# Optimization experiments

Hardware: AMD Instinct MI355X
Metric: run time of the kernel (lower is better)

## Reference

```python
import jax, jax.numpy as jnp
import numpy as np
from jax import lax

B, C, H, W = 8, 36, 256, 256
E, K, TD = 6, 2, 32
HID = C * 2  # ffn_expansion_factor = 2
EPS = 1e-10


def _conv3x3(x, w):
    # x: [B, Cin, H, W], w: [Cout, Cin, 3, 3], stride 1, pad 1, no bias
    return lax.conv_general_dilated(
        x, w, window_strides=(1, 1), padding=[(1, 1), (1, 1)],
        dimension_numbers=("NCHW", "OIHW", "NCHW"))


def _cv_squared(v):
    # torch .var() is unbiased (ddof=1)
    return jnp.var(v, ddof=1) / (jnp.mean(v) ** 2 + EPS)


def setup_inputs() -> dict:
    key = jax.random.key(0)
    ks = jax.random.split(key, 10)
    s = 0.05
    return {
        "x": jax.random.normal(ks[0], (B, C, H, W), dtype=jnp.float32),
        "time": jax.random.normal(ks[1], (B, TD), dtype=jnp.float32),
        # FeatureWiseAffine: Linear(time_dim -> expert_dim*2)
        "time_w": jax.random.normal(ks[2], (TD, HID), dtype=jnp.float32) * s,
        "time_b": jnp.zeros((HID,), dtype=jnp.float32),
        # gate: Linear(72,72) -> LeakyReLU -> Linear(72,6)
        "gate_w1": jax.random.normal(ks[3], (HID, HID), dtype=jnp.float32) * s,
        "gate_b1": jnp.zeros((HID,), dtype=jnp.float32),
        "gate_w2": jax.random.normal(ks[4], (HID, E), dtype=jnp.float32) * s,
        "gate_b2": jnp.zeros((E,), dtype=jnp.float32),
        # per-expert conv weights, stacked over experts
        "conv1_w": jax.random.normal(ks[5], (E, HID, C, 3, 3), dtype=jnp.float32) * s,
        "conv2_w": jax.random.normal(ks[6], (E, C, HID, 3, 3), dtype=jnp.float32) * s,
    }


def reference(x, time, time_w, time_b, gate_w1, gate_b1, gate_w2, gate_b2,
              conv1_w, conv2_w):
    # ---- gating (eval mode: no noise) ----
    # NOTE: source names are swapped: self.maxpool = AdaptiveAvgPool2d(1),
    # self.meanpool = AdaptiveMaxPool2d(1). Order preserved: [avg, max].
    avg_vec = jnp.mean(x, axis=(2, 3))              # [B, C]
    max_vec = jnp.max(x, axis=(2, 3))               # [B, C]
    v = jnp.concatenate([avg_vec, max_vec], axis=1)  # [B, 2C]
    v = v + time @ time_w + time_b                   # FeatureWiseAffine (additive)
    h = v @ gate_w1 + gate_b1
    h = jnp.where(h > 0, h, 0.01 * h)                # LeakyReLU(0.01)
    clean_logits = h @ gate_w2 + gate_b2             # [B, E]

    top_vals, top_idx = lax.top_k(clean_logits, min(K + 1, E))
    topk_gates = jax.nn.softmax(top_vals[:, :K], axis=1)     # [B, K]
    rows = jnp.arange(B)[:, None]
    gates = jnp.zeros_like(clean_logits).at[rows, top_idx[:, :K]].set(topk_gates)

    importance = gates.sum(axis=0)                           # [E]
    load = (gates > 0).sum(axis=0).astype(jnp.float32)       # [E] (eval path)
    loss = (_cv_squared(importance) + _cv_squared(load)) * 0.01

    # ---- dense equivalent of sparse dispatch / expert / gate-weighted combine ----
    # y[b] = sum_e gates[b,e] * expert_e(x[b]); zero gates contribute nothing,
    # identical to SparseDispatcher's gather -> conv -> scatter-add combine.
    y = jnp.zeros_like(x)
    for e in range(E):
        t = _conv3x3(x, conv1_w[e])
        t = jax.nn.gelu(t, approximate=False)   # F.gelu default = exact erf
        t = _conv3x3(t, conv2_w[e])
        y = y + gates[:, e].reshape(B, 1, 1, 1) * t
    return y, loss
```

## Files before the change

### kernel.cpp

```cpp
#include <hip/hip_runtime.h>
#include <hip/hip_bf16.h>
#include <math.h>

#define BB 8
#define CCH 36
#define HH 256
#define WW 256
#define EE 6
#define TDIM 32
#define HID 72
#define WS_GATES (BB*CCH*2)
#define WT1_OFF 4096
#define WT2_OFF (4096 + 368640)

#define TW 16
#define TH 8
#define XR 12
#define XC 20
#define TR 10
#define TC 18

typedef __attribute__((ext_vector_type(8))) short bf16x8;
typedef __attribute__((ext_vector_type(4))) float f32x4;

static __device__ __forceinline__ unsigned short f2bf(float f) {
  __hip_bfloat16 h = __float2bfloat16(f);
  return *(unsigned short*)&h;
}
static __device__ __forceinline__ float gelu_fast(float x) {
  float n2u = x * (-1.5957691216f - 0.0713548162f * x * x);
  float r = __builtin_amdgcn_rcpf(1.f + __expf(n2u));
  return x * r;
}

__global__ __launch_bounds__(256) void poolwx_kernel(const float* __restrict__ x,
                                                     const float* __restrict__ w1,
                                                     const float* __restrict__ w2,
                                                     float* __restrict__ ws,
                                                     unsigned short* __restrict__ wt1,
                                                     unsigned short* __restrict__ wt2) {
  if (blockIdx.x < 288) {
    const int bc = blockIdx.x;
    const float* p = x + (size_t)bc * (HH * WW);
    float s = 0.f, m = -INFINITY;
    for (int i = threadIdx.x; i < (HH * WW) / 4; i += 256) {
      float4 v = ((const float4*)p)[i];
      s += v.x + v.y + v.z + v.w;
      m = fmaxf(m, fmaxf(fmaxf(v.x, v.y), fmaxf(v.z, v.w)));
    }
    for (int off = 32; off; off >>= 1) {
      s += __shfl_down(s, off);
      m = fmaxf(m, __shfl_down(m, off));
    }
    __shared__ float ss[4], sm[4];
    int wid = threadIdx.x >> 6, lane = threadIdx.x & 63;
    if (lane == 0) { ss[wid] = s; sm[wid] = m; }
    __syncthreads();
    if (threadIdx.x == 0) {
      float S = ss[0] + ss[1] + ss[2] + ss[3];
      float M = fmaxf(fmaxf(sm[0], sm[1]), fmaxf(sm[2], sm[3]));
      ws[bc] = S * (1.f / (HH * WW));
      ws[BB * CCH + bc] = M;
    }
    return;
  }
  int i = (blockIdx.x - 288) * 256 + threadIdx.x;
  const int n1 = 360 * 512;
  if (i < n1) {
    int j = i & 7;
    int lane = (i >> 3) & 63;
    int f = i >> 9;
    int mt = f % 5;  f /= 5;
    int kc = f % 4;  f /= 4;
    int dx = f % 3;  int e = f / 3;
    int co = mt * 16 + (lane & 15);
    int k = kc * 32 + (lane >> 4) * 8 + j;
    int dy = k / 40, ci = k % 40;
    float v = 0.f;
    if (co < HID && k < 120 && ci < CCH)
      v = w1[(((size_t)(e * HID + co) * CCH + ci) * 3 + dy) * 3 + dx];
    wt1[i] = f2bf(v);
  }
  const int n2 = 378 * 512;
  if (i < n2) {
    int j = i & 7;
    int lane = (i >> 3) & 63;
    int f = i >> 9;
    int mt = f % 3;  f /= 3;
    int kc = f % 7;  f /= 7;
    int dx = f % 3;  int e = f / 3;
    int co = mt * 16 + (lane & 15);
    int k = kc * 32 + (lane >> 4) * 8 + j;
    int dy = k / 72, ci = k % 72;
    float v = 0.f;
    if (co < CCH && k < 216)
      v = w2[(((size_t)(e * CCH + co) * HID + ci) * 3 + dy) * 3 + dx];
    wt2[i] = f2bf(v);
  }
}

__global__ void gate_kernel(const float* __restrict__ time,
                            const float* __restrict__ time_w,
                            const float* __restrict__ time_b,
                            const float* __restrict__ w1, const float* __restrict__ b1,
                            const float* __restrict__ w2, const float* __restrict__ b2,
                            float* __restrict__ ws, float* __restrict__ loss_out) {
  __shared__ float v[BB * HID];
  __shared__ float h[BB * HID];
  __shared__ float logits[BB * EE];
  const int t = threadIdx.x;
  const float* avg = ws;
  const float* mx = ws + BB * CCH;
  for (int i = t; i < BB * HID; i += blockDim.x) {
    int b = i / HID, c = i % HID;
    float base = (c < CCH) ? avg[b * CCH + c] : mx[b * CCH + (c - CCH)];
    float acc = time_b[c];
    for (int k = 0; k < TDIM; k++) acc += time[b * TDIM + k] * time_w[k * HID + c];
    v[i] = base + acc;
  }
  __syncthreads();
  for (int i = t; i < BB * HID; i += blockDim.x) {
    int b = i / HID, c = i % HID;
    float acc = b1[c];
    for (int k = 0; k < HID; k++) acc += v[b * HID + k] * w1[k * HID + c];
    h[i] = acc > 0.f ? acc : 0.01f * acc;
  }
  __syncthreads();
  for (int i = t; i < BB * EE; i += blockDim.x) {
    int b = i / EE, e = i % EE;
    float acc = b2[e];
    for (int k = 0; k < HID; k++) acc += h[b * HID + k] * w2[k * EE + e];
    logits[i] = acc;
  }
  __syncthreads();
  if (t == 0) {
    float imp[EE], ld[EE];
    for (int e = 0; e < EE; e++) { imp[e] = 0.f; ld[e] = 0.f; }
    for (int b = 0; b < BB; b++) {
      int i1 = -1, i2 = -1;
      float v1 = -1e30f, v2 = -1e30f;
      for (int e = 0; e < EE; e++) {
        float lv = logits[b * EE + e];
        if (lv > v1) { v2 = v1; i2 = i1; v1 = lv; i1 = e; }
        else if (lv > v2) { v2 = lv; i2 = e; }
      }
      float e2 = expf(v2 - v1);
      float g1 = 1.f / (1.f + e2), g2 = e2 / (1.f + e2);
      for (int e = 0; e < EE; e++) ws[WS_GATES + b * EE + e] = 0.f;
      ws[WS_GATES + b * EE + i1] = g1;
      ws[WS_GATES + b * EE + i2] = g2;
      imp[i1] += g1; imp[i2] += g2;
      ld[i1] += 1.f; ld[i2] += 1.f;
    }
    float loss = 0.f;
    {
      float m = 0.f; for (int e = 0; e < EE; e++) m += imp[e]; m /= EE;
      float var = 0.f; for (int e = 0; e < EE; e++) { float d = imp[e] - m; var += d * d; }
      var /= (EE - 1);
      loss += var / (m * m + 1e-10f);
      m = 0.f; for (int e = 0; e < EE; e++) m += ld[e]; m /= EE;
      var = 0.f; for (int e = 0; e < EE; e++) { float d = ld[e] - m; var += d * d; }
      var /= (EE - 1);
      loss += var / (m * m + 1e-10f);
    }
    loss_out[0] = 0.01f * loss;
  }
}

__global__ __launch_bounds__(256, 3) void conv_kernel(
    const float* __restrict__ x,
    const unsigned short* __restrict__ wt1,
    const unsigned short* __restrict__ wt2,
    const float* __restrict__ wsg,
    float* __restrict__ y) {
  __shared__ __align__(16) char lds[48000];
  char* xsB = lds;
  char* tsB = lds + 19200;

  const int tid = threadIdx.x;
  const int w = tid >> 6;
  const int lane = tid & 63;
  const int l15 = lane & 15;
  const int kl = lane >> 4;
  const int b = blockIdx.y;
  const int tileId = (blockIdx.x & 7) * 64 + (blockIdx.x >> 3);
  const int tx0 = (tileId & 15) * TW;
  const int ty0 = (tileId >> 4) * TH;
  const size_t xbase = (size_t)b * (CCH * HH * WW);

  int eids[2] = {0, 0};
  float gvals[2] = {0.f, 0.f};
  int ne = 0;
  for (int e = 0; e < EE; e++) {
    float g = wsg[b * EE + e];
    if (g != 0.f && ne < 2) { eids[ne] = e; gvals[ne] = g; ne++; }
  }
  ne = __builtin_amdgcn_readfirstlane(ne);
  const int e0 = __builtin_amdgcn_readfirstlane(eids[0]);
  const int e1 = __builtin_amdgcn_readfirstlane(eids[1]);
  const float g0 = __int_as_float(__builtin_amdgcn_readfirstlane(__float_as_int(gvals[0])));
  const float g1 = __int_as_float(__builtin_amdgcn_readfirstlane(__float_as_int(gvals[1])));

  if (tid < XR * XC) {
    const int xr = tid / XC, xc = tid - (tid / XC) * XC;
    const int gy = ty0 - 2 + xr, gx = tx0 - 2 + xc;
    const bool valid = ((unsigned)gy < (unsigned)HH) && ((unsigned)gx < (unsigned)WW);
    const float* xp = x + xbase + (size_t)(gy * WW + gx);
    char* dstb = xsB + (xr * XC + xc) * 16;
#pragma unroll
    for (int c8 = 0; c8 < 5; c8++) {
      unsigned int pk[4];
#pragma unroll
      for (int q = 0; q < 4; q++) {
        int ci0 = c8 * 8 + q * 2, ci1 = ci0 + 1;
        float v0 = (ci0 < CCH && valid) ? xp[(size_t)ci0 << 16] : 0.f;
        float v1 = (ci1 < CCH && valid) ? xp[(size_t)ci1 << 16] : 0.f;
        pk[q] = (unsigned)f2bf(v0) | ((unsigned)f2bf(v1) << 16);
      }
      *(uint4*)(dstb + c8 * 3840) = make_uint4(pk[0], pk[1], pk[2], pk[3]);
    }
  }

  int vimg[3], pst[3], tsoff[3], pb1[3];
#pragma unroll
  for (int i = 0; i < 3; i++) {
    int p = (w + 4 * i) * 16 + l15;
    int tr = p / TC, tc = p - tr * TC;
    pst[i] = (p < TR * TC) ? 1 : 0;
    int trc = tr < (TR - 1) ? tr : (TR - 1);
    pb1[i] = trc * 320 + tc * 16;
    tsoff[i] = trc * 288 + tc * 16;
    int gy = ty0 - 1 + tr, gx = tx0 - 1 + tc;
    vimg[i] = (pst[i] && (unsigned)gy < (unsigned)HH && (unsigned)gx < (unsigned)WW) ? 1 : 0;
  }
  int b1a[4][3];
#pragma unroll
  for (int kc = 0; kc < 4; kc++) {
    int k0 = kc * 32 + kl * 8;
    int d = (k0 >= 80) ? 2 : (k0 >= 40 ? 1 : 0);
    int xkc = (k0 < 120) ? (((k0 - 40 * d) >> 3) * 3840 + d * 320) : 0;
#pragma unroll
    for (int i = 0; i < 3; i++) b1a[kc][i] = pb1[i] + xkc;
  }
  int tsStore[3];
#pragma unroll
  for (int i = 0; i < 3; i++) tsStore[i] = tsoff[i] + (kl >> 1) * 2880 + (kl & 1) * 8;

  int b2a[7][2];
#pragma unroll
  for (int kc = 0; kc < 7; kc++) {
    int k0 = kc * 32 + kl * 8;
    int d = (k0 >= 144) ? 2 : (k0 >= 72 ? 1 : 0);
    int tkc = (k0 < 216) ? (((k0 - 72 * d) >> 3) * 2880 + d * 288) : 0;
#pragma unroll
    for (int i = 0; i < 2; i++) b2a[kc][i] = (w + 4 * i) * 288 + l15 * 16 + tkc;
  }

  const int lob = lane * 8;

  f32x4 yacc[2][3];
#pragma unroll
  for (int i = 0; i < 2; i++)
#pragma unroll
    for (int mt = 0; mt < 3; mt++) yacc[i][mt] = (f32x4){0.f, 0.f, 0.f, 0.f};

  __syncthreads();

#pragma unroll
  for (int ei = 0; ei < 2; ei++) {
    if (ei >= ne) break;
    const float gv = ei ? g1 : g0;
    const unsigned short* w1p = wt1 + (ei ? e1 : e0) * 30720;
    const unsigned short* w2p = wt2 + (ei ? e1 : e0) * 32256;

    f32x4 acc[3][5];
#pragma unroll
    for (int i = 0; i < 3; i++)
#pragma unroll
      for (int mt = 0; mt < 5; mt++) acc[i][mt] = (f32x4){0.f, 0.f, 0.f, 0.f};

    bf16x8 aA[5], aB[5];
#pragma unroll
    for (int mt = 0; mt < 5; mt++) aA[mt] = *(const bf16x8*)(w1p + mt * 512 + lob);

#pragma unroll
    for (int jj = 0; jj < 12; jj++) {
      if (jj < 11) {
#pragma unroll
        for (int mt = 0; mt < 5; mt++)
          ((jj & 1) ? aA : aB)[mt] = *(const bf16x8*)(w1p + ((jj + 1) * 5 + mt) * 512 + lob);
      }
      const int kc = jj & 3;
      const int dxo = (jj >> 2) * 16;
      bf16x8 bv[3];
#pragma unroll
      for (int i = 0; i < 3; i++)
        bv[i] = *(const bf16x8*)(xsB + b1a[kc][i] + dxo);
      __builtin_amdgcn_s_setprio(1);
#pragma unroll
      for (int mt = 0; mt < 5; mt++) {
        bf16x8 av = ((jj & 1) ? aB : aA)[mt];
#pragma unroll
        for (int i = 0; i < 3; i++)
          acc[i][mt] = __builtin_amdgcn_mfma_f32_16x16x32_bf16(av, bv[i], acc[i][mt], 0, 0, 0);
      }
      __builtin_amdgcn_s_setprio(0);
    }

    bf16x8 cA[3], cB[3];
#pragma unroll
    for (int mt = 0; mt < 3; mt++) cA[mt] = *(const bf16x8*)(w2p + mt * 512 + lob);

#pragma unroll
    for (int i = 0; i < 3; i++) {
      if (pst[i]) {
#pragma unroll
        for (int mt = 0; mt < 5; mt++) {
          float v0 = vimg[i] ? gelu_fast(acc[i][mt].x) : 0.f;
          float v1 = vimg[i] ? gelu_fast(acc[i][mt].y) : 0.f;
          float v2 = vimg[i] ? gelu_fast(acc[i][mt].z) : 0.f;
          float v3 = vimg[i] ? gelu_fast(acc[i][mt].w) : 0.f;
          unsigned int lo = (unsigned)f2bf(v0) | ((unsigned)f2bf(v1) << 16);
          unsigned int hi = (unsigned)f2bf(v2) | ((unsigned)f2bf(v3) << 16);
          *(uint2*)(tsB + tsStore[i] + mt * 5760) = make_uint2(lo, hi);
        }
      }
    }
    __syncthreads();

    f32x4 acc2[2][3];
#pragma unroll
    for (int i = 0; i < 2; i++)
#pragma unroll
      for (int mt = 0; mt < 3; mt++) acc2[i][mt] = (f32x4){0.f, 0.f, 0.f, 0.f};

#pragma unroll
    for (int jj = 0; jj < 21; jj++) {
      if (jj < 20) {
#pragma unroll
        for (int mt = 0; mt < 3; mt++)
          ((jj & 1) ? cA : cB)[mt] = *(const bf16x8*)(w2p + ((jj + 1) * 3 + mt) * 512 + lob);
      }
      const int kc = jj % 7;
      const int dxo = (jj / 7) * 16;
      bf16x8 bv[2];
#pragma unroll
      for (int i = 0; i < 2; i++)
        bv[i] = *(const bf16x8*)(tsB + b2a[kc][i] + dxo);
      __builtin_amdgcn_s_setprio(1);
#pragma unroll
      for (int mt = 0; mt < 3; mt++) {
        bf16x8 av = ((jj & 1) ? cB : cA)[mt];
#pragma unroll
        for (int i = 0; i < 2; i++)
          acc2[i][mt] = __builtin_amdgcn_mfma_f32_16x16x32_bf16(av, bv[i], acc2[i][mt], 0, 0, 0);
      }
      __builtin_amdgcn_s_setprio(0);
    }
#pragma unroll
    for (int i = 0; i < 2; i++)
#pragma unroll
      for (int mt = 0; mt < 3; mt++) yacc[i][mt] += gv * acc2[i][mt];
    __syncthreads();
  }

#pragma unroll
  for (int i = 0; i < 2; i++) {
    int row = w + 4 * i;
#pragma unroll
    for (int mt = 0; mt < 3; mt++) {
#pragma unroll
      for (int r = 0; r < 4; r++) {
        int co = mt * 16 + kl * 4 + r;
        if (co < CCH) {
          float v = (r == 0) ? yacc[i][mt].x : (r == 1) ? yacc[i][mt].y
                  : (r == 2) ? yacc[i][mt].z : yacc[i][mt].w;
          y[xbase + ((size_t)co << 16) + (size_t)((ty0 + row) * WW + tx0 + l15)] = v;
        }
      }
    }
  }
}

extern "C" void kernel_launch(void* const* d_in, const int* in_sizes, int n_in,
                              void* d_out, int out_size, void* d_ws, size_t ws_size,
                              hipStream_t stream) {
  const float* x      = (const float*)d_in[0];
  const float* time   = (const float*)d_in[1];
  const float* time_w = (const float*)d_in[2];
  const float* time_b = (const float*)d_in[3];
  const float* gw1    = (const float*)d_in[4];
  const float* gb1    = (const float*)d_in[5];
  const float* gw2    = (const float*)d_in[6];
  const float* gb2    = (const float*)d_in[7];
  const float* w1     = (const float*)d_in[8];
  const float* w2     = (const float*)d_in[9];
  float* out = (float*)d_out;
  float* ws  = (float*)d_ws;
  unsigned short* wt1 = (unsigned short*)((char*)d_ws + WT1_OFF);
  unsigned short* wt2 = (unsigned short*)((char*)d_ws + WT2_OFF);

  hipLaunchKernelGGL(poolwx_kernel, dim3(288 + 756), dim3(256), 0, stream,
                     x, w1, w2, ws, wt1, wt2);
  hipLaunchKernelGGL(gate_kernel, dim3(1), dim3(128), 0, stream,
                     time, time_w, time_b, gw1, gb1, gw2, gb2,
                     ws, out + (size_t)(out_size - 1));
  hipLaunchKernelGGL(conv_kernel, dim3(512, BB), dim3(256), 0, stream,
                     x, wt1, wt2, ws + WS_GATES, out);
}
```

Baseline: 238.7 us.

## Deepen weight prefetch and fold gate scaling into conv2 accumulation

Conv1 and conv2 weight fragments are now prefetched across whole dx or kc groups rather than double-buffered one step ahead, so global weight loads have more MFMA work to hide behind. The gate value is applied to the GELU output before bf16 packing, which lets conv2 accumulate straight into yacc and drops the separate acc2 registers and scale-add. The cost is a larger register footprint for the fragments, which may lower occupancy, and scaling by the gate before bf16 rounding changes rounding slightly.

```diff
diff --git a/kernel.cpp b/kernel.cpp
--- a/kernel.cpp
+++ b/kernel.cpp
@@ -279,47 +279,53 @@
 #pragma unroll
       for (int mt = 0; mt < 5; mt++) acc[i][mt] = (f32x4){0.f, 0.f, 0.f, 0.f};
 
-    bf16x8 aA[5], aB[5];
-#pragma unroll
-    for (int mt = 0; mt < 5; mt++) aA[mt] = *(const bf16x8*)(w1p + mt * 512 + lob);
-
-#pragma unroll
-    for (int jj = 0; jj < 12; jj++) {
-      if (jj < 11) {
-#pragma unroll
-        for (int mt = 0; mt < 5; mt++)
-          ((jj & 1) ? aA : aB)[mt] = *(const bf16x8*)(w1p + ((jj + 1) * 5 + mt) * 512 + lob);
-      }
-      const int kc = jj & 3;
-      const int dxo = (jj >> 2) * 16;
-      bf16x8 bv[3];
-#pragma unroll
-      for (int i = 0; i < 3; i++)
-        bv[i] = *(const bf16x8*)(xsB + b1a[kc][i] + dxo);
-      __builtin_amdgcn_s_setprio(1);
-#pragma unroll
-      for (int mt = 0; mt < 5; mt++) {
-        bf16x8 av = ((jj & 1) ? aB : aA)[mt];
+    bf16x8 f1[3][5];
+#pragma unroll
+    for (int dx = 0; dx < 3; dx++)
+#pragma unroll
+      for (int mt = 0; mt < 5; mt++)
+        f1[dx][mt] = *(const bf16x8*)(w1p + (dx * 4) * 5 * 512 + mt * 512 + lob);
+
+#pragma unroll
+    for (int kc = 0; kc < 4; kc++) {
+#pragma unroll
+      for (int dx = 0; dx < 3; dx++) {
+        bf16x8 bv[3];
 #pragma unroll
         for (int i = 0; i < 3; i++)
-          acc[i][mt] = __builtin_amdgcn_mfma_f32_16x16x32_bf16(av, bv[i], acc[i][mt], 0, 0, 0);
-      }
-      __builtin_amdgcn_s_setprio(0);
-    }
-
-    bf16x8 cA[3], cB[3];
-#pragma unroll
-    for (int mt = 0; mt < 3; mt++) cA[mt] = *(const bf16x8*)(w2p + mt * 512 + lob);
+          bv[i] = *(const bf16x8*)(xsB + b1a[kc][i] + dx * 16);
+        __builtin_amdgcn_s_setprio(1);
+#pragma unroll
+        for (int mt = 0; mt < 5; mt++) {
+#pragma unroll
+          for (int i = 0; i < 3; i++)
+            acc[i][mt] = __builtin_amdgcn_mfma_f32_16x16x32_bf16(f1[dx][mt], bv[i], acc[i][mt], 0, 0, 0);
+        }
+        __builtin_amdgcn_s_setprio(0);
+        if (kc < 3) {
+#pragma unroll
+          for (int mt = 0; mt < 5; mt++)
+            f1[dx][mt] = *(const bf16x8*)(w1p + ((dx * 4 + kc + 1) * 5 + mt) * 512 + lob);
+        }
+      }
+    }
+
+    bf16x8 f2[7][3];
+#pragma unroll
+    for (int kc = 0; kc < 7; kc++)
+#pragma unroll
+      for (int mt = 0; mt < 3; mt++)
+        f2[kc][mt] = *(const bf16x8*)(w2p + (kc * 3 + mt) * 512 + lob);
 
 #pragma unroll
     for (int i = 0; i < 3; i++) {
       if (pst[i]) {
 #pragma unroll
         for (int mt = 0; mt < 5; mt++) {
-          float v0 = vimg[i] ? gelu_fast(acc[i][mt].x) : 0.f;
-          float v1 = vimg[i] ? gelu_fast(acc[i][mt].y) : 0.f;
-          float v2 = vimg[i] ? gelu_fast(acc[i][mt].z) : 0.f;
-          float v3 = vimg[i] ? gelu_fast(acc[i][mt].w) : 0.f;
+          float v0 = vimg[i] ? gv * gelu_fast(acc[i][mt].x) : 0.f;
+          float v1 = vimg[i] ? gv * gelu_fast(acc[i][mt].y) : 0.f;
+          float v2 = vimg[i] ? gv * gelu_fast(acc[i][mt].z) : 0.f;
+          float v3 = vimg[i] ? gv * gelu_fast(acc[i][mt].w) : 0.f;
           unsigned int lo = (unsigned)f2bf(v0) | ((unsigned)f2bf(v1) << 16);
           unsigned int hi = (unsigned)f2bf(v2) | ((unsigned)f2bf(v3) << 16);
           *(uint2*)(tsB + tsStore[i] + mt * 5760) = make_uint2(lo, hi);
@@ -328,39 +334,26 @@
     }
     __syncthreads();
 
-    f32x4 acc2[2][3];
-#pragma unroll
-    for (int i = 0; i < 2; i++)
-#pragma unroll
-      for (int mt = 0; mt < 3; mt++) acc2[i][mt] = (f32x4){0.f, 0.f, 0.f, 0.f};
-
-#pragma unroll
-    for (int jj = 0; jj < 21; jj++) {
-      if (jj < 20) {
-#pragma unroll
-        for (int mt = 0; mt < 3; mt++)
-          ((jj & 1) ? cA : cB)[mt] = *(const bf16x8*)(w2p + ((jj + 1) * 3 + mt) * 512 + lob);
-      }
-      const int kc = jj % 7;
-      const int dxo = (jj / 7) * 16;
-      bf16x8 bv[2];
-#pragma unroll
-      for (int i = 0; i < 2; i++)
-        bv[i] = *(const bf16x8*)(tsB + b2a[kc][i] + dxo);
-      __builtin_amdgcn_s_setprio(1);
-#pragma unroll
-      for (int mt = 0; mt < 3; mt++) {
-        bf16x8 av = ((jj & 1) ? cB : cA)[mt];
-#pragma unroll
-        for (int i = 0; i < 2; i++)
-          acc2[i][mt] = __builtin_amdgcn_mfma_f32_16x16x32_bf16(av, bv[i], acc2[i][mt], 0, 0, 0);
-      }
-      __builtin_amdgcn_s_setprio(0);
-    }
-#pragma unroll
-    for (int i = 0; i < 2; i++)
-#pragma unroll
-      for (int mt = 0; mt < 3; mt++) yacc[i][mt] += gv * acc2[i][mt];
+#pragma unroll
+    for (int dx = 0; dx < 3; dx++) {
+#pragma unroll
+      for (int kc = 0; kc < 7; kc++) {
+        bf16x8 bv0 = *(const bf16x8*)(tsB + b2a[kc][0] + dx * 16);
+        bf16x8 bv1 = *(const bf16x8*)(tsB + b2a[kc][1] + dx * 16);
+        __builtin_amdgcn_s_setprio(1);
+#pragma unroll
+        for (int mt = 0; mt < 3; mt++) {
+          yacc[0][mt] = __builtin_amdgcn_mfma_f32_16x16x32_bf16(f2[kc][mt], bv0, yacc[0][mt], 0, 0, 0);
+          yacc[1][mt] = __builtin_amdgcn_mfma_f32_16x16x32_bf16(f2[kc][mt], bv1, yacc[1][mt], 0, 0, 0);
+        }
+        __builtin_amdgcn_s_setprio(0);
+        if (dx < 2) {
+#pragma unroll
+          for (int mt = 0; mt < 3; mt++)
+            f2[kc][mt] = *(const bf16x8*)(w2p + (((dx + 1) * 7 + kc) * 3 + mt) * 512 + lob);
+        }
+      }
+    }
     __syncthreads();
   }
 
```

After: 300.6 us. +25.9%, slower.

## Double conv tile height to 16 rows and fold gate weight into GELU output

Applied to the files above, without the earlier changes.

Grows each conv block's output tile from 16x8 to 16x16 pixels, halving the block count. Each block now covers more pixels per weight fragment load, and the 2-pixel halo is recomputed less often relative to the tile. The gate scale moves into the GELU stage, so the second conv accumulates straight into the output accumulators, and the mostly padding upper half of the last 16-channel hidden chunk is no longer written to LDS. This needs about 78KB of LDS and many more accumulator registers, so occupancy falls from 3 to 2 blocks per CU and register spills are possible.

```diff
diff --git a/kernel.cpp b/kernel.cpp
--- a/kernel.cpp
+++ b/kernel.cpp
@@ -14,11 +14,15 @@
 #define WT2_OFF (4096 + 368640)
 
 #define TW 16
-#define TH 8
-#define XR 12
+#define TH 16
+#define XR 20
 #define XC 20
-#define TR 10
+#define TR 18
 #define TC 18
+#define XROW 320
+#define XCHUNK 6400
+#define TROW 288
+#define TCHUNK 5184
 
 typedef __attribute__((ext_vector_type(8))) short bf16x8;
 typedef __attribute__((ext_vector_type(4))) float f32x4;
@@ -167,15 +171,15 @@
   }
 }
 
-__global__ __launch_bounds__(256, 3) void conv_kernel(
+__global__ __launch_bounds__(256, 2) void conv_kernel(
     const float* __restrict__ x,
     const unsigned short* __restrict__ wt1,
     const unsigned short* __restrict__ wt2,
     const float* __restrict__ wsg,
     float* __restrict__ y) {
-  __shared__ __align__(16) char lds[48000];
+  __shared__ __align__(16) char lds[78656];
   char* xsB = lds;
-  char* tsB = lds + 19200;
+  char* tsB = lds + 32000;
 
   const int tid = threadIdx.x;
   const int w = tid >> 6;
@@ -183,7 +187,7 @@
   const int l15 = lane & 15;
   const int kl = lane >> 4;
   const int b = blockIdx.y;
-  const int tileId = (blockIdx.x & 7) * 64 + (blockIdx.x >> 3);
+  const int tileId = (blockIdx.x & 7) * 32 + (blockIdx.x >> 3);
   const int tx0 = (tileId & 15) * TW;
   const int ty0 = (tileId >> 4) * TH;
   const size_t xbase = (size_t)b * (CCH * HH * WW);
@@ -201,66 +205,55 @@
   const float g0 = __int_as_float(__builtin_amdgcn_readfirstlane(__float_as_int(gvals[0])));
   const float g1 = __int_as_float(__builtin_amdgcn_readfirstlane(__float_as_int(gvals[1])));
 
-  if (tid < XR * XC) {
-    const int xr = tid / XC, xc = tid - (tid / XC) * XC;
-    const int gy = ty0 - 2 + xr, gx = tx0 - 2 + xc;
-    const bool valid = ((unsigned)gy < (unsigned)HH) && ((unsigned)gx < (unsigned)WW);
-    const float* xp = x + xbase + (size_t)(gy * WW + gx);
-    char* dstb = xsB + (xr * XC + xc) * 16;
-#pragma unroll
-    for (int c8 = 0; c8 < 5; c8++) {
-      unsigned int pk[4];
-#pragma unroll
-      for (int q = 0; q < 4; q++) {
-        int ci0 = c8 * 8 + q * 2, ci1 = ci0 + 1;
-        float v0 = (ci0 < CCH && valid) ? xp[(size_t)ci0 << 16] : 0.f;
-        float v1 = (ci1 < CCH && valid) ? xp[(size_t)ci1 << 16] : 0.f;
-        pk[q] = (unsigned)f2bf(v0) | ((unsigned)f2bf(v1) << 16);
-      }
-      *(uint4*)(dstb + c8 * 3840) = make_uint4(pk[0], pk[1], pk[2], pk[3]);
-    }
-  }
-
-  int vimg[3], pst[3], tsoff[3], pb1[3];
-#pragma unroll
-  for (int i = 0; i < 3; i++) {
+#pragma unroll
+  for (int it = 0; it < 2; it++) {
+    int pidx = tid + it * 256;
+    if (pidx < XR * XC) {
+      const int xr = pidx / XC, xc = pidx - (pidx / XC) * XC;
+      const int gy = ty0 - 2 + xr, gx = tx0 - 2 + xc;
+      const bool valid = ((unsigned)gy < (unsigned)HH) && ((unsigned)gx < (unsigned)WW);
+      const float* xp = x + xbase + (size_t)(gy * WW + gx);
+      char* dstb = xsB + pidx * 16;
+#pragma unroll
+      for (int c8 = 0; c8 < 5; c8++) {
+        unsigned int pk[4];
+#pragma unroll
+        for (int q = 0; q < 4; q++) {
+          int ci0 = c8 * 8 + q * 2, ci1 = ci0 + 1;
+          float v0 = (ci0 < CCH && valid) ? xp[(size_t)ci0 << 16] : 0.f;
+          float v1 = (ci1 < CCH && valid) ? xp[(size_t)ci1 << 16] : 0.f;
+          pk[q] = (unsigned)f2bf(v0) | ((unsigned)f2bf(v1) << 16);
+        }
+        *(uint4*)(dstb + c8 * XCHUNK) = make_uint4(pk[0], pk[1], pk[2], pk[3]);
+      }
+    }
+  }
+
+  int vimg[6], pst[6], pb1[6], tsoff[6];
+#pragma unroll
+  for (int i = 0; i < 6; i++) {
     int p = (w + 4 * i) * 16 + l15;
-    int tr = p / TC, tc = p - tr * TC;
+    int tr = p / TC, tc = p - (p / TC) * TC;
     pst[i] = (p < TR * TC) ? 1 : 0;
     int trc = tr < (TR - 1) ? tr : (TR - 1);
-    pb1[i] = trc * 320 + tc * 16;
-    tsoff[i] = trc * 288 + tc * 16;
+    pb1[i] = trc * XROW + tc * 16;
+    tsoff[i] = trc * TROW + tc * 16 + (kl >> 1) * TCHUNK + (kl & 1) * 8;
     int gy = ty0 - 1 + tr, gx = tx0 - 1 + tc;
     vimg[i] = (pst[i] && (unsigned)gy < (unsigned)HH && (unsigned)gx < (unsigned)WW) ? 1 : 0;
   }
-  int b1a[4][3];
+  int xkc[4];
 #pragma unroll
   for (int kc = 0; kc < 4; kc++) {
     int k0 = kc * 32 + kl * 8;
     int d = (k0 >= 80) ? 2 : (k0 >= 40 ? 1 : 0);
-    int xkc = (k0 < 120) ? (((k0 - 40 * d) >> 3) * 3840 + d * 320) : 0;
-#pragma unroll
-    for (int i = 0; i < 3; i++) b1a[kc][i] = pb1[i] + xkc;
-  }
-  int tsStore[3];
-#pragma unroll
-  for (int i = 0; i < 3; i++) tsStore[i] = tsoff[i] + (kl >> 1) * 2880 + (kl & 1) * 8;
-
-  int b2a[7][2];
-#pragma unroll
-  for (int kc = 0; kc < 7; kc++) {
-    int k0 = kc * 32 + kl * 8;
-    int d = (k0 >= 144) ? 2 : (k0 >= 72 ? 1 : 0);
-    int tkc = (k0 < 216) ? (((k0 - 72 * d) >> 3) * 2880 + d * 288) : 0;
-#pragma unroll
-    for (int i = 0; i < 2; i++) b2a[kc][i] = (w + 4 * i) * 288 + l15 * 16 + tkc;
+    xkc[kc] = (k0 < 120) ? (((k0 - 40 * d) >> 3) * XCHUNK + d * XROW) : 0;
   }
 
   const int lob = lane * 8;
 
-  f32x4 yacc[2][3];
-#pragma unroll
-  for (int i = 0; i < 2; i++)
+  f32x4 yacc[4][3];
+#pragma unroll
+  for (int i = 0; i < 4; i++)
 #pragma unroll
     for (int mt = 0; mt < 3; mt++) yacc[i][mt] = (f32x4){0.f, 0.f, 0.f, 0.f};
 
@@ -273,9 +266,9 @@
     const unsigned short* w1p = wt1 + (ei ? e1 : e0) * 30720;
     const unsigned short* w2p = wt2 + (ei ? e1 : e0) * 32256;
 
-    f32x4 acc[3][5];
-#pragma unroll
-    for (int i = 0; i < 3; i++)
+    f32x4 acc[6][5];
+#pragma unroll
+    for (int i = 0; i < 6; i++)
 #pragma unroll
       for (int mt = 0; mt < 5; mt++) acc[i][mt] = (f32x4){0.f, 0.f, 0.f, 0.f};
 
@@ -292,16 +285,16 @@
       }
       const int kc = jj & 3;
       const int dxo = (jj >> 2) * 16;
-      bf16x8 bv[3];
-#pragma unroll
-      for (int i = 0; i < 3; i++)
-        bv[i] = *(const bf16x8*)(xsB + b1a[kc][i] + dxo);
+      bf16x8 bv[6];
+#pragma unroll
+      for (int i = 0; i < 6; i++)
+        bv[i] = *(const bf16x8*)(xsB + pb1[i] + xkc[kc] + dxo);
       __builtin_amdgcn_s_setprio(1);
 #pragma unroll
       for (int mt = 0; mt < 5; mt++) {
         bf16x8 av = ((jj & 1) ? aB : aA)[mt];
 #pragma unroll
-        for (int i = 0; i < 3; i++)
+        for (int i = 0; i < 6; i++)
           acc[i][mt] = __builtin_amdgcn_mfma_f32_16x16x32_bf16(av, bv[i], acc[i][mt], 0, 0, 0);
       }
       __builtin_amdgcn_s_setprio(0);
@@ -312,27 +305,34 @@
     for (int mt = 0; mt < 3; mt++) cA[mt] = *(const bf16x8*)(w2p + mt * 512 + lob);
 
 #pragma unroll
-    for (int i = 0; i < 3; i++) {
+    for (int i = 0; i < 6; i++) {
       if (pst[i]) {
 #pragma unroll
         for (int mt = 0; mt < 5; mt++) {
-          float v0 = vimg[i] ? gelu_fast(acc[i][mt].x) : 0.f;
-          float v1 = vimg[i] ? gelu_fast(acc[i][mt].y) : 0.f;
-          float v2 = vimg[i] ? gelu_fast(acc[i][mt].z) : 0.f;
-          float v3 = vimg[i] ? gelu_fast(acc[i][mt].w) : 0.f;
-          unsigned int lo = (unsigned)f2bf(v0) | ((unsigned)f2bf(v1) << 16);
-          unsigned int hi = (unsigned)f2bf(v2) | ((unsigned)f2bf(v3) << 16);
-          *(uint2*)(tsB + tsStore[i] + mt * 5760) = make_uint2(lo, hi);
+          if (mt < 4 || kl < 2) {
+            float v0 = vimg[i] ? gv * gelu_fast(acc[i][mt].x) : 0.f;
+            float v1 = vimg[i] ? gv * gelu_fast(acc[i][mt].y) : 0.f;
+            float v2 = vimg[i] ? gv * gelu_fast(acc[i][mt].z) : 0.f;
+            float v3 = vimg[i] ? gv * gelu_fast(acc[i][mt].w) : 0.f;
+            unsigned int lo = (unsigned)f2bf(v0) | ((unsigned)f2bf(v1) << 16);
+            unsigned int hi = (unsigned)f2bf(v2) | ((unsigned)f2bf(v3) << 16);
+            *(uint2*)(tsB + tsoff[i] + mt * (2 * TCHUNK)) = make_uint2(lo, hi);
+          }
         }
       }
     }
     __syncthreads();
 
-    f32x4 acc2[2][3];
-#pragma unroll
-    for (int i = 0; i < 2; i++)
-#pragma unroll
-      for (int mt = 0; mt < 3; mt++) acc2[i][mt] = (f32x4){0.f, 0.f, 0.f, 0.f};
+    int tkc[7];
+#pragma unroll
+    for (int kc = 0; kc < 7; kc++) {
+      int k0 = kc * 32 + kl * 8;
+      int d = (k0 >= 144) ? 2 : (k0 >= 72 ? 1 : 0);
+      tkc[kc] = (k0 < 216) ? (((k0 - 72 * d) >> 3) * TCHUNK + d * TROW) : 0;
+    }
+    int pb2[4];
+#pragma unroll
+    for (int i = 0; i < 4; i++) pb2[i] = (w + 4 * i) * TROW + l15 * 16;
 
 #pragma unroll
     for (int jj = 0; jj < 21; jj++) {
@@ -343,29 +343,25 @@
       }
       const int kc = jj % 7;
       const int dxo = (jj / 7) * 16;
-      bf16x8 bv[2];
-#pragma unroll
-      for (int i = 0; i < 2; i++)
-        bv[i] = *(const bf16x8*)(tsB + b2a[kc][i] + dxo);
+      bf16x8 bv[4];
+#pragma unroll
+      for (int i = 0; i < 4; i++)
+        bv[i] = *(const bf16x8*)(tsB + pb2[i] + tkc[kc] + dxo);
       __builtin_amdgcn_s_setprio(1);
 #pragma unroll
       for (int mt = 0; mt < 3; mt++) {
         bf16x8 av = ((jj & 1) ? cB : cA)[mt];
 #pragma unroll
-        for (int i = 0; i < 2; i++)
-          acc2[i][mt] = __builtin_amdgcn_mfma_f32_16x16x32_bf16(av, bv[i], acc2[i][mt], 0, 0, 0);
+        for (int i = 0; i < 4; i++)
+          yacc[i][mt] = __builtin_amdgcn_mfma_f32_16x16x32_bf16(av, bv[i], yacc[i][mt], 0, 0, 0);
       }
       __builtin_amdgcn_s_setprio(0);
     }
-#pragma unroll
-    for (int i = 0; i < 2; i++)
-#pragma unroll
-      for (int mt = 0; mt < 3; mt++) yacc[i][mt] += gv * acc2[i][mt];
     __syncthreads();
   }
 
 #pragma unroll
-  for (int i = 0; i < 2; i++) {
+  for (int i = 0; i < 4; i++) {
     int row = w + 4 * i;
 #pragma unroll
     for (int mt = 0; mt < 3; mt++) {
@@ -405,6 +401,6 @@
   hipLaunchKernelGGL(gate_kernel, dim3(1), dim3(128), 0, stream,
                      time, time_w, time_b, gw1, gb1, gw2, gb2,
                      ws, out + (size_t)(out_size - 1));
-  hipLaunchKernelGGL(conv_kernel, dim3(512, BB), dim3(256), 0, stream,
+  hipLaunchKernelGGL(conv_kernel, dim3(256, BB), dim3(256), 0, stream,
                      x, wt1, wt2, ws + WS_GATES, out);
 }
```

Result: slower. 271.8 us (+13.8%).
